# Kernel optimization log

Measured on AMD Instinct MI355X. Metric: run time of the kernel, lower is better.

The kernel has to match this reference:

```python
import jax, jax.numpy as jnp
import numpy as np

NHEAD = 8  # from init_kwargs
EPS = 1e-5  # nn.LayerNorm default


def _ln(x, w, b):
    mu = jnp.mean(x, axis=-1, keepdims=True)
    var = jnp.mean(jnp.square(x - mu), axis=-1, keepdims=True)
    return (x - mu) * jax.lax.rsqrt(var + EPS) * w + b


def setup_inputs() -> dict:
    key = jax.random.key(0)
    L, D, FF, B, S = 4, 256, 512, 2, 4096
    ks = jax.random.split(key, 14)
    s = 0.02
    inp = {
        "seq": jax.random.normal(ks[0], (B, S, D), jnp.float32),
        "Wqkv": jax.random.normal(ks[1], (L, 3 * D, D), jnp.float32) * s,
        "bqkv": jnp.zeros((L, 3 * D), jnp.float32),
        "Wo": jax.random.normal(ks[2], (L, D, D), jnp.float32) * s,
        "bo": jnp.zeros((L, D), jnp.float32),
        "ln1_w": jnp.ones((L, D), jnp.float32),
        "ln1_b": jnp.zeros((L, D), jnp.float32),
        "ln2_w": jnp.ones((L, D), jnp.float32),
        "ln2_b": jnp.zeros((L, D), jnp.float32),
        "W1": jax.random.normal(ks[3], (L, FF, D), jnp.float32) * s,
        "b1": jnp.zeros((L, FF), jnp.float32),
        "W2": jax.random.normal(ks[4], (L, D, FF), jnp.float32) * s,
        "b2": jnp.zeros((L, D), jnp.float32),
        "n_ctx": 2048,
    }
    return inp


def _forward(seq, Wqkv, bqkv, Wo, bo, ln1_w, ln1_b, ln2_w, ln2_b, W1, b1, W2, b2, n_ctx):
    B, S, D = seq.shape
    H = NHEAD
    hd = D // H
    scale = 1.0 / np.sqrt(hd).astype(np.float32)
    x = seq
    L = Wqkv.shape[0]
    for l in range(L):
        # pre-norm self-attention block (norm_first=True)
        h = _ln(x, ln1_w[l], ln1_b[l])
        qkv = h @ Wqkv[l].T + bqkv[l]            # [B,S,3D]
        q, k, v = jnp.split(qkv, 3, axis=-1)
        q = q.reshape(B, S, H, hd)
        # Mask structure: every token (context AND query) may only attend to
        # context keys [:n_ctx] -> keys/values restricted up-front, no dense
        # [S,S] score matrix and no explicit mask needed.
        kc = k[:, :n_ctx].reshape(B, n_ctx, H, hd)
        vc = v[:, :n_ctx].reshape(B, n_ctx, H, hd)
        scores = jnp.einsum('bqhd,bkhd->bhqk', q, kc) * scale  # [B,H,S,n_ctx]
        att = jax.nn.softmax(scores, axis=-1)
        o = jnp.einsum('bhqk,bkhd->bqhd', att, vc).reshape(B, S, D)
        x = x + o @ Wo[l].T + bo[l]
        # pre-norm feed-forward block, exact (erf) GELU as in PyTorch 'gelu'
        h2 = _ln(x, ln2_w[l], ln2_b[l])
        x = x + jax.nn.gelu(h2 @ W1[l].T + b1[l], approximate=False) @ W2[l].T + b2[l]
    return x


def reference(seq, Wqkv, bqkv, Wo, bo, ln1_w, ln1_b, ln2_w, ln2_b, W1, b1, W2, b2, n_ctx):
    return _forward(seq, Wqkv, bqkv, Wo, bo, ln1_w, ln1_b, ln2_w, ln2_b, W1, b1, W2, b2, n_ctx)
```

## Files before the change

### kernel.cpp

```cpp
#include <hip/hip_runtime.h>
#include <hip/hip_bf16.h>

#define BB 2
#define SS 4096
#define DD 256
#define FFD 512
#define NLAYER 4
#define NHEAD 8
#define HD 32
#define QKVD 768
#define NROWS 8192
#define NCTX 2048

typedef unsigned short u16;
typedef unsigned int   u32;
typedef __attribute__((ext_vector_type(8))) short short8;
typedef __attribute__((ext_vector_type(4))) short sv4;
typedef __attribute__((ext_vector_type(4))) float f32x4;

#if __has_builtin(__builtin_amdgcn_exp2f)
#define EXP2(x) __builtin_amdgcn_exp2f(x)
#else
#define EXP2(x) exp2f(x)
#endif

__device__ __forceinline__ float bf2f(u32 u) { return __uint_as_float(u << 16); }
__device__ __forceinline__ u16 f2bu(float f) {
    union { __hip_bfloat16 h; u16 u; } cv; cv.h = __float2bfloat16(f); return cv.u;
}
__device__ __forceinline__ float gelu_f(float v) {
    return 0.5f * v * (1.0f + erff(v * 0.70710678118654752f));
}

__global__ void copy_kernel(const float* __restrict__ in, float* __restrict__ out, int n) {
    int i = (blockIdx.x * blockDim.x + threadIdx.x) * 4;
    if (i >= n) return;
    *reinterpret_cast<float4*>(out + i) = *reinterpret_cast<const float4*>(in + i);
}

__global__ void f2bw4_kernel(const float* __restrict__ s0, const float* __restrict__ s1,
                             const float* __restrict__ s2, const float* __restrict__ s3,
                             u16* __restrict__ d0, u16* __restrict__ d1,
                             u16* __restrict__ d2, u16* __restrict__ d3) {
    int blk = blockIdx.x;
    const float* s; u16* d; int base;
    if (blk < 768)       { s = s0; d = d0; base = blk; }
    else if (blk < 1024) { s = s1; d = d1; base = blk - 768; }
    else if (blk < 1536) { s = s2; d = d2; base = blk - 1024; }
    else                 { s = s3; d = d3; base = blk - 1536; }
    int i = (base * 256 + threadIdx.x) * 4;
    float4 v = *reinterpret_cast<const float4*>(s + i);
    uint2 o;
    o.x = (u32)f2bu(v.x) | ((u32)f2bu(v.y) << 16);
    o.y = (u32)f2bu(v.z) | ((u32)f2bu(v.w) << 16);
    *reinterpret_cast<uint2*>(d + i) = o;
}

__global__ void ln_kernel(const float* __restrict__ x, const float* __restrict__ w,
                          const float* __restrict__ b, u16* __restrict__ out) {
    int row = blockIdx.x * 4 + (threadIdx.x >> 6);
    int lane = threadIdx.x & 63;
    int c = lane * 4;
    float4 v = *reinterpret_cast<const float4*>(x + (size_t)row * DD + c);
    float s  = v.x + v.y + v.z + v.w;
    float sq = v.x*v.x + v.y*v.y + v.z*v.z + v.w*v.w;
    #pragma unroll
    for (int off = 32; off >= 1; off >>= 1) {
        s  += __shfl_xor(s, off);
        sq += __shfl_xor(sq, off);
    }
    float mu   = s * (1.0f / DD);
    float var  = sq * (1.0f / DD) - mu * mu;
    float rstd = rsqrtf(var + 1e-5f);
    float4 wv = *reinterpret_cast<const float4*>(w + c);
    float4 bv = *reinterpret_cast<const float4*>(b + c);
    float o0 = (v.x - mu) * rstd * wv.x + bv.x;
    float o1 = (v.y - mu) * rstd * wv.y + bv.y;
    float o2 = (v.z - mu) * rstd * wv.z + bv.z;
    float o3 = (v.w - mu) * rstd * wv.w + bv.w;
    uint2 o;
    o.x = (u32)f2bu(o0) | ((u32)f2bu(o1) << 16);
    o.y = (u32)f2bu(o2) | ((u32)f2bu(o3) << 16);
    *reinterpret_cast<uint2*>(out + (size_t)row * DD + c) = o;
}

template<int TM, int ACT, int RES>
__global__ __launch_bounds__(256) void mfma_gemm(
        const u16* __restrict__ A, const u16* __restrict__ W, const float* __restrict__ bias,
        float* __restrict__ outf, u16* __restrict__ outb, int N, int K) {
    constexpr int MI = TM / 32;
    __shared__ __align__(16) u16 As[TM][136];
    __shared__ __align__(16) u16 Ws[64][136];
    int tid = threadIdx.x;
    int wave = tid >> 6, lane = tid & 63, la = lane & 15, quad = lane >> 4;
    int wm = (wave & 1) * (TM / 2), wn = (wave >> 1) * 32;
    int m0 = blockIdx.y * TM, n0 = blockIdx.x * 64;
    f32x4 acc[MI][2];
    #pragma unroll
    for (int mi = 0; mi < MI; mi++)
        #pragma unroll
        for (int ni = 0; ni < 2; ni++)
            acc[mi][ni] = (f32x4){0.f, 0.f, 0.f, 0.f};

    int ar = tid >> 4, ac = (tid & 15) * 8;
    for (int k0 = 0; k0 < K; k0 += 128) {
        #pragma unroll
        for (int p = 0; p < TM / 16; p++)
            *reinterpret_cast<uint4*>(&As[ar + p*16][ac]) =
                *reinterpret_cast<const uint4*>(&A[(size_t)(m0 + ar + p*16) * K + k0 + ac]);
        #pragma unroll
        for (int p = 0; p < 4; p++)
            *reinterpret_cast<uint4*>(&Ws[ar + p*16][ac]) =
                *reinterpret_cast<const uint4*>(&W[(size_t)(n0 + ar + p*16) * K + k0 + ac]);
        __syncthreads();
        #pragma unroll
        for (int kh = 0; kh < 4; kh++) {
            short8 af[MI], bf[2];
            #pragma unroll
            for (int mi = 0; mi < MI; mi++)
                af[mi] = *reinterpret_cast<const short8*>(&As[wm + mi*16 + la][kh*32 + quad*8]);
            #pragma unroll
            for (int ni = 0; ni < 2; ni++)
                bf[ni] = *reinterpret_cast<const short8*>(&Ws[wn + ni*16 + la][kh*32 + quad*8]);
            #pragma unroll
            for (int mi = 0; mi < MI; mi++)
                #pragma unroll
                for (int ni = 0; ni < 2; ni++)
                    acc[mi][ni] = __builtin_amdgcn_mfma_f32_16x16x32_bf16(af[mi], bf[ni], acc[mi][ni], 0, 0, 0);
        }
        __syncthreads();
    }

    #pragma unroll
    for (int mi = 0; mi < MI; mi++) {
        #pragma unroll
        for (int ni = 0; ni < 2; ni++) {
            int n = n0 + wn + ni*16 + la;
            float bv = bias[n];
            #pragma unroll
            for (int r = 0; r < 4; r++) {
                int m = m0 + wm + mi*16 + quad*4 + r;
                float v = acc[mi][ni][r] + bv;
                if (ACT) v = gelu_f(v);
                if (RES) outf[(size_t)m * N + n] += v;
                else     outb[(size_t)m * N + n] = f2bu(v);
            }
        }
    }
}

__global__ __launch_bounds__(256) void vtrans_kernel(const u16* __restrict__ qkv,
                                                     u16* __restrict__ vtg) {
    __shared__ __align__(16) u16 T[32][68];
    int tid = threadIdx.x;
    int kt = blockIdx.x, bh = blockIdx.y;
    int b = bh >> 3, hh = bh & 7;
    int key = tid >> 2, hd8 = (tid & 3) * 8;
    uint4 u = *reinterpret_cast<const uint4*>(
        &qkv[((size_t)b * SS + kt*64 + key) * QKVD + 2*DD + hh*32 + hd8]);
    int lowk = key & 31;
    int pos = (key & 32) | (((lowk >> 2) & 3) << 3) | (((lowk >> 4) & 1) << 2) | (lowk & 3);
    T[hd8 + 0][pos] = (u16)(u.x);  T[hd8 + 1][pos] = (u16)(u.x >> 16);
    T[hd8 + 2][pos] = (u16)(u.y);  T[hd8 + 3][pos] = (u16)(u.y >> 16);
    T[hd8 + 4][pos] = (u16)(u.z);  T[hd8 + 5][pos] = (u16)(u.z >> 16);
    T[hd8 + 6][pos] = (u16)(u.w);  T[hd8 + 7][pos] = (u16)(u.w >> 16);
    __syncthreads();
    int row = tid >> 3, cg = (tid & 7) * 8;
    sv4 lo = *reinterpret_cast<const sv4*>(&T[row][cg]);
    sv4 hi = *reinterpret_cast<const sv4*>(&T[row][cg + 4]);
    union { sv4 a[2]; uint4 u4; } cvt; cvt.a[0] = lo; cvt.a[1] = hi;
    *reinterpret_cast<uint4*>(&vtg[((size_t)bh*32 + row) * NCTX + kt*64 + cg]) = cvt.u4;
}

#define SCL2 0.2550437f
#define SH2  11.5415603f
__global__ __launch_bounds__(512, 4) void mfma_attn(const u16* __restrict__ qkv,
                                                    const u16* __restrict__ vtg,
                                                    u16* __restrict__ out) {
    __shared__ __align__(16) u16 smem[9728];
    u16 (*Ks)[64][40] = reinterpret_cast<u16(*)[64][40]>(smem);
    u16 (*Vt)[32][72] = reinterpret_cast<u16(*)[32][72]>(smem + 5120);

    int tid = threadIdx.x;
    int wv = tid >> 6, lane = tid & 63, la = lane & 15, quad = lane >> 4;
    int qw = wv & 3, ksp = wv >> 2;
    int bh = blockIdx.y, qidx = blockIdx.x;
    int b = bh >> 3, hh = bh & 7;
    size_t tokbase = (size_t)b * SS;
    int qb = qidx * 128 + qw * 32;

    short8 qf[2];
    #pragma unroll
    for (int qt = 0; qt < 2; qt++) {
        uint4 u = *reinterpret_cast<const uint4*>(
            &qkv[(tokbase + qb + qt*16 + la) * QKVD + hh*32 + quad*8]);
        union { short8 v; u16 e[8]; } qa;
        u32 w[4] = {u.x, u.y, u.z, u.w};
        #pragma unroll
        for (int i = 0; i < 4; i++) {
            qa.e[2*i]   = f2bu(bf2f(w[i] & 0xffffu) * SCL2);
            qa.e[2*i+1] = f2bu(bf2f(w[i] >> 16) * SCL2);
        }
        qf[qt] = qa.v;
    }

    f32x4 o[2][2];
    #pragma unroll
    for (int i = 0; i < 2; i++)
        #pragma unroll
        for (int j = 0; j < 2; j++) o[i][j] = (f32x4){0.f, 0.f, 0.f, 0.f};
    f32x4 l_acc[2];
    l_acc[0] = (f32x4){0.f, 0.f, 0.f, 0.f};
    l_acc[1] = (f32x4){0.f, 0.f, 0.f, 0.f};
    const f32x4 cinit = (f32x4){-SH2, -SH2, -SH2, -SH2};
    short8 onesf;
    { union { short8 v; u16 e[8]; } t;
      #pragma unroll
      for (int i = 0; i < 8; i++) t.e[i] = 0x3F80;
      onesf = t.v; }

    int sr = tid >> 2, sk = (tid & 3) * 8;
    int hs = sr >> 6, krow = sr & 63;
    int vr = tid >> 4, vc = (tid & 15) * 8;
    int vh = vc >> 6, vcol = vc & 63;
    const u16* kgp = &qkv[(tokbase + hs*1024 + krow) * QKVD + DD + hh*32 + sk];
    const u16* vgp = &vtg[((size_t)bh*32 + vr) * NCTX + vh*1024 + vcol];
    uint4 kreg = *reinterpret_cast<const uint4*>(kgp);
    uint4 vreg = *reinterpret_cast<const uint4*>(vgp);

    for (int step = 0; step < 16; step++) {
        *reinterpret_cast<uint4*>(&Ks[hs][krow][sk]) = kreg;
        *reinterpret_cast<uint4*>(&Vt[vh][vr][vcol]) = vreg;
        __syncthreads();
        if (step < 15) {
            kreg = *reinterpret_cast<const uint4*>(kgp + (size_t)(step+1)*64*QKVD);
            vreg = *reinterpret_cast<const uint4*>(vgp + (step+1)*64);
        }

        #pragma unroll
        for (int c = 0; c < 2; c++) {
            short8 kf0 = *reinterpret_cast<const short8*>(&Ks[ksp][c*32 + la][quad*8]);
            short8 kf1 = *reinterpret_cast<const short8*>(&Ks[ksp][c*32 + 16 + la][quad*8]);
            f32x4 s00 = __builtin_amdgcn_mfma_f32_16x16x32_bf16(kf0, qf[0], cinit, 0, 0, 0);
            f32x4 s10 = __builtin_amdgcn_mfma_f32_16x16x32_bf16(kf1, qf[0], cinit, 0, 0, 0);
            f32x4 s01 = __builtin_amdgcn_mfma_f32_16x16x32_bf16(kf0, qf[1], cinit, 0, 0, 0);
            f32x4 s11 = __builtin_amdgcn_mfma_f32_16x16x32_bf16(kf1, qf[1], cinit, 0, 0, 0);

            union { uint4 u; short8 v; } pf0, pf1;
            {
                u32 a0 = __float_as_uint(EXP2(s00[0])), a1 = __float_as_uint(EXP2(s00[1]));
                u32 a2 = __float_as_uint(EXP2(s00[2])), a3 = __float_as_uint(EXP2(s00[3]));
                u32 b0 = __float_as_uint(EXP2(s10[0])), b1 = __float_as_uint(EXP2(s10[1]));
                u32 b2 = __float_as_uint(EXP2(s10[2])), b3 = __float_as_uint(EXP2(s10[3]));
                pf0.u.x = __builtin_amdgcn_perm(a1, a0, 0x07060302u);
                pf0.u.y = __builtin_amdgcn_perm(a3, a2, 0x07060302u);
                pf0.u.z = __builtin_amdgcn_perm(b1, b0, 0x07060302u);
                pf0.u.w = __builtin_amdgcn_perm(b3, b2, 0x07060302u);
            }
            {
                u32 a0 = __float_as_uint(EXP2(s01[0])), a1 = __float_as_uint(EXP2(s01[1]));
                u32 a2 = __float_as_uint(EXP2(s01[2])), a3 = __float_as_uint(EXP2(s01[3]));
                u32 b0 = __float_as_uint(EXP2(s11[0])), b1 = __float_as_uint(EXP2(s11[1]));
                u32 b2 = __float_as_uint(EXP2(s11[2])), b3 = __float_as_uint(EXP2(s11[3]));
                pf1.u.x = __builtin_amdgcn_perm(a1, a0, 0x07060302u);
                pf1.u.y = __builtin_amdgcn_perm(a3, a2, 0x07060302u);
                pf1.u.z = __builtin_amdgcn_perm(b1, b0, 0x07060302u);
                pf1.u.w = __builtin_amdgcn_perm(b3, b2, 0x07060302u);
            }

            l_acc[0] = __builtin_amdgcn_mfma_f32_16x16x32_bf16(onesf, pf0.v, l_acc[0], 0, 0, 0);
            l_acc[1] = __builtin_amdgcn_mfma_f32_16x16x32_bf16(onesf, pf1.v, l_acc[1], 0, 0, 0);

            short8 vf0 = *reinterpret_cast<const short8*>(&Vt[ksp][la][c*32 + quad*8]);
            short8 vf1 = *reinterpret_cast<const short8*>(&Vt[ksp][16 + la][c*32 + quad*8]);
            o[0][0] = __builtin_amdgcn_mfma_f32_16x16x32_bf16(vf0, pf0.v, o[0][0], 0, 0, 0);
            o[0][1] = __builtin_amdgcn_mfma_f32_16x16x32_bf16(vf0, pf1.v, o[0][1], 0, 0, 0);
            o[1][0] = __builtin_amdgcn_mfma_f32_16x16x32_bf16(vf1, pf0.v, o[1][0], 0, 0, 0);
            o[1][1] = __builtin_amdgcn_mfma_f32_16x16x32_bf16(vf1, pf1.v, o[1][1], 0, 0, 0);
        }
        __syncthreads();
    }

    float* obuf = reinterpret_cast<float*>(smem);
    if (wv >= 4) {
        int idx = (qw * 64 + lane) * 18;
        #pragma unroll
        for (int mio = 0; mio < 2; mio++)
            #pragma unroll
            for (int qt = 0; qt < 2; qt++)
                #pragma unroll
                for (int r = 0; r < 4; r++)
                    obuf[idx + mio*8 + qt*4 + r] = o[mio][qt][r];
        obuf[idx + 16] = l_acc[0][0];
        obuf[idx + 17] = l_acc[1][0];
    }
    __syncthreads();
    if (wv < 4) {
        int idx = (qw * 64 + lane) * 18;
        #pragma unroll
        for (int mio = 0; mio < 2; mio++)
            #pragma unroll
            for (int qt = 0; qt < 2; qt++)
                #pragma unroll
                for (int r = 0; r < 4; r++)
                    o[mio][qt][r] += obuf[idx + mio*8 + qt*4 + r];
        float liq[2];
        liq[0] = 1.0f / (l_acc[0][0] + obuf[idx + 16]);
        liq[1] = 1.0f / (l_acc[1][0] + obuf[idx + 17]);
        #pragma unroll
        for (int qt = 0; qt < 2; qt++) {
            float li = liq[qt];
            size_t token = tokbase + qb + qt*16 + la;
            #pragma unroll
            for (int mio = 0; mio < 2; mio++) {
                uint2 w;
                w.x = (u32)f2bu(o[mio][qt][0] * li) | ((u32)f2bu(o[mio][qt][1] * li) << 16);
                w.y = (u32)f2bu(o[mio][qt][2] * li) | ((u32)f2bu(o[mio][qt][3] * li) << 16);
                *reinterpret_cast<uint2*>(&out[token * DD + hh*32 + mio*16 + quad*4]) = w;
            }
        }
    }
}

extern "C" void kernel_launch(void* const* d_in, const int* in_sizes, int n_in,
                              void* d_out, int out_size, void* d_ws, size_t ws_size,
                              hipStream_t stream) {
    const float* seq   = (const float*)d_in[0];
    const float* Wqkv  = (const float*)d_in[1];
    const float* bqkv  = (const float*)d_in[2];
    const float* Wo    = (const float*)d_in[3];
    const float* bo    = (const float*)d_in[4];
    const float* ln1w  = (const float*)d_in[5];
    const float* ln1b  = (const float*)d_in[6];
    const float* ln2w  = (const float*)d_in[7];
    const float* ln2b  = (const float*)d_in[8];
    const float* W1    = (const float*)d_in[9];
    const float* b1    = (const float*)d_in[10];
    const float* W2    = (const float*)d_in[11];
    const float* b2    = (const float*)d_in[12];

    const int NX = NROWS * DD;
    float* x    = (float*)d_out;
    char* wsb   = (char*)d_ws;
    u16*  qkv   = (u16*)wsb;
    u16*  ff    = qkv;
    u16*  h     = (u16*)(wsb + 12582912);
    u16*  hln   = (u16*)(wsb + 16777216);
    u16*  wbf   = (u16*)(wsb + 20971520);
    u16*  vtg   = (u16*)(wsb + 25165824);
    u16* wqkv_b = wbf;
    u16* wo_b   = wbf + 786432;
    u16* w1_b   = wbf + 1048576;
    u16* w2_b   = wbf + 1572864;

    f2bw4_kernel<<<2048, 256, 0, stream>>>(Wqkv, Wo, W1, W2, wqkv_b, wo_b, w1_b, w2_b);
    copy_kernel<<<NX/1024, 256, 0, stream>>>(seq, x, NX);

    for (int l = 0; l < NLAYER; l++) {
        ln_kernel<<<NROWS/4, 256, 0, stream>>>(x, ln1w + l*DD, ln1b + l*DD, hln);
        mfma_gemm<128,0,0><<<dim3(QKVD/64, NROWS/128), 256, 0, stream>>>(
            hln, wqkv_b + (size_t)l*QKVD*DD, bqkv + l*QKVD, nullptr, qkv, QKVD, DD);
        vtrans_kernel<<<dim3(NCTX/64, BB*NHEAD), 256, 0, stream>>>(qkv, vtg);
        mfma_attn<<<dim3(SS/128, BB*NHEAD), 512, 0, stream>>>(qkv, vtg, h);
        mfma_gemm<64,0,1><<<dim3(DD/64, NROWS/64), 256, 0, stream>>>(
            h, wo_b + (size_t)l*DD*DD, bo + l*DD, x, nullptr, DD, DD);
        ln_kernel<<<NROWS/4, 256, 0, stream>>>(x, ln2w + l*DD, ln2b + l*DD, hln);
        mfma_gemm<128,1,0><<<dim3(FFD/64, NROWS/128), 256, 0, stream>>>(
            hln, w1_b + (size_t)l*FFD*DD, b1 + l*FFD, nullptr, ff, FFD, DD);
        mfma_gemm<64,0,1><<<dim3(DD/64, NROWS/64), 256, 0, stream>>>(
            ff, w2_b + (size_t)l*DD*FFD, b2 + l*DD, x, nullptr, DD, FFD);
    }
}
```

Baseline: 401.9 us.

## Use direct global-to-LDS loads with XOR swizzle, remap workgroups, double-buffer attention tiles

The GEMM now stages A and W tiles with global_load_lds (direct global-to-LDS DMA) into unpadded LDS rows, using an XOR swizzle on 16-byte column groups to avoid bank conflicts in place of padding. Both the GEMM and attention kernels remap the flat block index so that consecutive blocks are spread across XCD groups, aiming for better L2 locality. The attention kernel double-buffers its K/V LDS tiles, removing one barrier per step and prefetching two steps ahead, at the cost of twice the LDS, which may lower occupancy. The direct-LDS load addressing relies on per-wave contiguous placement and is subtle to get right.

```diff
diff --git a/kernel.cpp b/kernel.cpp
--- a/kernel.cpp
+++ b/kernel.cpp
@@ -30,6 +30,12 @@
 }
 __device__ __forceinline__ float gelu_f(float v) {
     return 0.5f * v * (1.0f + erff(v * 0.70710678118654752f));
+}
+
+typedef const __attribute__((address_space(1))) u32* gas1p;
+typedef __attribute__((address_space(3))) u32* las3p;
+__device__ __forceinline__ void gload_lds16(void* lds, const void* g) {
+    __builtin_amdgcn_global_load_lds((gas1p)g, (las3p)lds, 16, 0, 0);
 }
 
 __global__ void copy_kernel(const float* __restrict__ in, float* __restrict__ out, int n) {
@@ -89,12 +95,18 @@
         const u16* __restrict__ A, const u16* __restrict__ W, const float* __restrict__ bias,
         float* __restrict__ outf, u16* __restrict__ outb, int N, int K) {
     constexpr int MI = TM / 32;
-    __shared__ __align__(16) u16 As[TM][136];
-    __shared__ __align__(16) u16 Ws[64][136];
+    __shared__ __align__(16) u16 As[TM][128];
+    __shared__ __align__(16) u16 Ws[64][128];
     int tid = threadIdx.x;
     int wave = tid >> 6, lane = tid & 63, la = lane & 15, quad = lane >> 4;
     int wm = (wave & 1) * (TM / 2), wn = (wave >> 1) * 32;
-    int m0 = blockIdx.y * TM, n0 = blockIdx.x * 64;
+
+    int nwg = gridDim.x * gridDim.y;
+    int flat = blockIdx.y * gridDim.x + blockIdx.x;
+    int f2 = (flat & 7) * (nwg >> 3) + (flat >> 3);
+    int bx = f2 % gridDim.x, by = f2 / gridDim.x;
+    int m0 = by * TM, n0 = bx * 64;
+
     f32x4 acc[MI][2];
     #pragma unroll
     for (int mi = 0; mi < MI; mi++)
@@ -102,26 +114,37 @@
         for (int ni = 0; ni < 2; ni++)
             acc[mi][ni] = (f32x4){0.f, 0.f, 0.f, 0.f};
 
-    int ar = tid >> 4, ac = (tid & 15) * 8;
+    int srow = tid >> 4;
+    int sg   = tid & 15;
     for (int k0 = 0; k0 < K; k0 += 128) {
         #pragma unroll
-        for (int p = 0; p < TM / 16; p++)
-            *reinterpret_cast<uint4*>(&As[ar + p*16][ac]) =
-                *reinterpret_cast<const uint4*>(&A[(size_t)(m0 + ar + p*16) * K + k0 + ac]);
-        #pragma unroll
-        for (int p = 0; p < 4; p++)
-            *reinterpret_cast<uint4*>(&Ws[ar + p*16][ac]) =
-                *reinterpret_cast<const uint4*>(&W[(size_t)(n0 + ar + p*16) * K + k0 + ac]);
+        for (int p = 0; p < TM / 16; p++) {
+            int row = p * 16 + srow;
+            gload_lds16(&As[p * 16 + (wave << 2)][0],
+                        &A[(size_t)(m0 + row) * K + k0 + ((sg ^ (row & 7)) << 3)]);
+        }
+        #pragma unroll
+        for (int p = 0; p < 4; p++) {
+            int row = p * 16 + srow;
+            gload_lds16(&Ws[p * 16 + (wave << 2)][0],
+                        &W[(size_t)(n0 + row) * K + k0 + ((sg ^ (row & 7)) << 3)]);
+        }
         __syncthreads();
         #pragma unroll
         for (int kh = 0; kh < 4; kh++) {
             short8 af[MI], bf[2];
             #pragma unroll
-            for (int mi = 0; mi < MI; mi++)
-                af[mi] = *reinterpret_cast<const short8*>(&As[wm + mi*16 + la][kh*32 + quad*8]);
-            #pragma unroll
-            for (int ni = 0; ni < 2; ni++)
-                bf[ni] = *reinterpret_cast<const short8*>(&Ws[wn + ni*16 + la][kh*32 + quad*8]);
+            for (int mi = 0; mi < MI; mi++) {
+                int row = wm + mi * 16 + la;
+                af[mi] = *reinterpret_cast<const short8*>(
+                    &As[row][((kh * 4 + quad) ^ (row & 7)) << 3]);
+            }
+            #pragma unroll
+            for (int ni = 0; ni < 2; ni++) {
+                int row = wn + ni * 16 + la;
+                bf[ni] = *reinterpret_cast<const short8*>(
+                    &Ws[row][((kh * 4 + quad) ^ (row & 7)) << 3]);
+            }
             #pragma unroll
             for (int mi = 0; mi < MI; mi++)
                 #pragma unroll
@@ -177,14 +200,16 @@
 __global__ __launch_bounds__(512, 4) void mfma_attn(const u16* __restrict__ qkv,
                                                     const u16* __restrict__ vtg,
                                                     u16* __restrict__ out) {
-    __shared__ __align__(16) u16 smem[9728];
-    u16 (*Ks)[64][40] = reinterpret_cast<u16(*)[64][40]>(smem);
-    u16 (*Vt)[32][72] = reinterpret_cast<u16(*)[32][72]>(smem + 5120);
+    __shared__ __align__(16) u16 smem[19456];
+    u16 (*Ks)[2][64][40] = reinterpret_cast<u16(*)[2][64][40]>(smem);
+    u16 (*Vt)[2][32][72] = reinterpret_cast<u16(*)[2][32][72]>(smem + 10240);
 
     int tid = threadIdx.x;
     int wv = tid >> 6, lane = tid & 63, la = lane & 15, quad = lane >> 4;
     int qw = wv & 3, ksp = wv >> 2;
-    int bh = blockIdx.y, qidx = blockIdx.x;
+    int flat = blockIdx.y * gridDim.x + blockIdx.x;
+    int f2 = (flat & 7) * 64 + (flat >> 3);
+    int qidx = f2 & 31, bh = f2 >> 5;
     int b = bh >> 3, hh = bh & 7;
     size_t tokbase = (size_t)b * SS;
     int qb = qidx * 128 + qw * 32;
@@ -225,22 +250,30 @@
     int vh = vc >> 6, vcol = vc & 63;
     const u16* kgp = &qkv[(tokbase + hs*1024 + krow) * QKVD + DD + hh*32 + sk];
     const u16* vgp = &vtg[((size_t)bh*32 + vr) * NCTX + vh*1024 + vcol];
+
     uint4 kreg = *reinterpret_cast<const uint4*>(kgp);
     uint4 vreg = *reinterpret_cast<const uint4*>(vgp);
+    *reinterpret_cast<uint4*>(&Ks[0][hs][krow][sk]) = kreg;
+    *reinterpret_cast<uint4*>(&Vt[0][vh][vr][vcol]) = vreg;
+    kreg = *reinterpret_cast<const uint4*>(kgp + (size_t)64*QKVD);
+    vreg = *reinterpret_cast<const uint4*>(vgp + 64);
+    __syncthreads();
 
     for (int step = 0; step < 16; step++) {
-        *reinterpret_cast<uint4*>(&Ks[hs][krow][sk]) = kreg;
-        *reinterpret_cast<uint4*>(&Vt[vh][vr][vcol]) = vreg;
-        __syncthreads();
+        int cur = step & 1;
         if (step < 15) {
-            kreg = *reinterpret_cast<const uint4*>(kgp + (size_t)(step+1)*64*QKVD);
-            vreg = *reinterpret_cast<const uint4*>(vgp + (step+1)*64);
+            *reinterpret_cast<uint4*>(&Ks[cur^1][hs][krow][sk]) = kreg;
+            *reinterpret_cast<uint4*>(&Vt[cur^1][vh][vr][vcol]) = vreg;
+            if (step < 14) {
+                kreg = *reinterpret_cast<const uint4*>(kgp + (size_t)(step+2)*64*QKVD);
+                vreg = *reinterpret_cast<const uint4*>(vgp + (step+2)*64);
+            }
         }
 
         #pragma unroll
         for (int c = 0; c < 2; c++) {
-            short8 kf0 = *reinterpret_cast<const short8*>(&Ks[ksp][c*32 + la][quad*8]);
-            short8 kf1 = *reinterpret_cast<const short8*>(&Ks[ksp][c*32 + 16 + la][quad*8]);
+            short8 kf0 = *reinterpret_cast<const short8*>(&Ks[cur][ksp][c*32 + la][quad*8]);
+            short8 kf1 = *reinterpret_cast<const short8*>(&Ks[cur][ksp][c*32 + 16 + la][quad*8]);
             f32x4 s00 = __builtin_amdgcn_mfma_f32_16x16x32_bf16(kf0, qf[0], cinit, 0, 0, 0);
             f32x4 s10 = __builtin_amdgcn_mfma_f32_16x16x32_bf16(kf1, qf[0], cinit, 0, 0, 0);
             f32x4 s01 = __builtin_amdgcn_mfma_f32_16x16x32_bf16(kf0, qf[1], cinit, 0, 0, 0);
@@ -271,8 +304,8 @@
             l_acc[0] = __builtin_amdgcn_mfma_f32_16x16x32_bf16(onesf, pf0.v, l_acc[0], 0, 0, 0);
             l_acc[1] = __builtin_amdgcn_mfma_f32_16x16x32_bf16(onesf, pf1.v, l_acc[1], 0, 0, 0);
 
-            short8 vf0 = *reinterpret_cast<const short8*>(&Vt[ksp][la][c*32 + quad*8]);
-            short8 vf1 = *reinterpret_cast<const short8*>(&Vt[ksp][16 + la][c*32 + quad*8]);
+            short8 vf0 = *reinterpret_cast<const short8*>(&Vt[cur][ksp][la][c*32 + quad*8]);
+            short8 vf1 = *reinterpret_cast<const short8*>(&Vt[cur][ksp][16 + la][c*32 + quad*8]);
             o[0][0] = __builtin_amdgcn_mfma_f32_16x16x32_bf16(vf0, pf0.v, o[0][0], 0, 0, 0);
             o[0][1] = __builtin_amdgcn_mfma_f32_16x16x32_bf16(vf0, pf1.v, o[0][1], 0, 0, 0);
             o[1][0] = __builtin_amdgcn_mfma_f32_16x16x32_bf16(vf1, pf0.v, o[1][0], 0, 0, 0);
```

Result: slower. 412.9 us (+2.7%).
